# Performance work log

Hardware: AMD Instinct MI355X
Metric: run time of the kernel (lower is better)

## Reference

```python
import jax, jax.numpy as jnp
import numpy as np

N_NODES = 100000
N_EDGES = 800000
N_GRAPHS = 16
NFEAT = 128
NHID = 128
NCLASS = 2


def setup_inputs() -> dict:
    key = jax.random.key(0)
    k1, k2, k3, k4, k5, k6, k7 = jax.random.split(key, 7)
    x = jax.random.normal(k1, (N_NODES, NFEAT), dtype=jnp.float32)
    edge_index = jax.random.randint(k2, (2, N_EDGES), 0, N_NODES, dtype=jnp.int64)
    batch = jnp.sort(jax.random.randint(k3, (N_NODES,), 0, N_GRAPHS, dtype=jnp.int64))
    # GCNConv params (glorot-ish scale)
    W1 = jax.random.normal(k4, (NFEAT, NHID), dtype=jnp.float32) / np.sqrt(NFEAT)
    b1 = jnp.zeros((NHID,), dtype=jnp.float32)
    W2 = jax.random.normal(k5, (NHID, NCLASS), dtype=jnp.float32) / np.sqrt(NHID)
    b2 = jnp.zeros((NCLASS,), dtype=jnp.float32)
    return {"x": x, "edge_index": edge_index, "batch": batch,
            "W1": W1, "b1": b1, "W2": W2, "b2": b2}


def _prep_edges(edge_index, n):
    """Add self-loops and compute symmetric GCN normalization."""
    loop = jnp.arange(n, dtype=edge_index.dtype)
    row = jnp.concatenate([edge_index[0], loop])  # source
    col = jnp.concatenate([edge_index[1], loop])  # target
    deg = jax.ops.segment_sum(jnp.ones_like(col, dtype=jnp.float32), col, num_segments=n)
    dinv = jnp.where(deg > 0, jax.lax.rsqrt(deg), 0.0)
    norm = dinv[row] * dinv[col]  # [E+N]
    return row, col, norm


def _gcn_conv(x, row, col, norm, W, b):
    h = x @ W                                  # [N, out]
    msg = h[row] * norm[:, None]               # gather + scale, [E+N, out]
    out = jax.ops.segment_sum(msg, col, num_segments=x.shape[0])  # scatter-add
    return out + b


def reference(x, edge_index, batch, W1, b1, W2, b2):
    n = x.shape[0]
    row, col, norm = _prep_edges(edge_index, n)
    h = jax.nn.relu(_gcn_conv(x, row, col, norm, W1, b1))
    # dropout is identity at inference
    h = _gcn_conv(h, row, col, norm, W2, b2)
    # global_mean_pool over graph ids
    sums = jax.ops.segment_sum(h, batch, num_segments=N_GRAPHS)          # [G, nclass]
    cnts = jax.ops.segment_sum(jnp.ones((n,), h.dtype), batch, num_segments=N_GRAPHS)
    pooled = sums / jnp.maximum(cnts, 1.0)[:, None]
    return jax.nn.log_softmax(pooled, axis=1)
```

## Files before the change

kernel.cpp:

```cpp
#include <hip/hip_runtime.h>
#include <hip/hip_bf16.h>

#define N_NODES 100000
#define N_EDGES 800000
#define N_GRAPHS 16
#define NFEAT 128
#define NHID 128
#define NCLASS 2

#define GEMM_BLOCKS 512
#define N_CHUNKS (N_NODES / 16)

#define FILL_BINS 8
#define FILL_SLICES 128
#define FILL_BIN_W (N_NODES / FILL_BINS)
#define FILL_SLICE_E (N_EDGES / FILL_SLICES)

#define SLOT_CAP 64
#define ZROW N_NODES

#define P2E_BLOCKS 1024
#define P2E_TPB 256

typedef unsigned int uint32;
typedef __attribute__((ext_vector_type(8))) short short8;
typedef __attribute__((ext_vector_type(4))) float f32x4;
typedef __attribute__((ext_vector_type(2))) float f32x2;

__device__ __forceinline__ unsigned short f2bf(float f) {
  __hip_bfloat16 h = __float2bfloat16(f);
  unsigned short r;
  __builtin_memcpy(&r, &h, 2);
  return r;
}

__global__ __launch_bounds__(256) void k_fill(const int* __restrict__ ei,
                                              int* __restrict__ deg,
                                              int* __restrict__ slots,
                                              unsigned char* __restrict__ xw8) {
  if (blockIdx.x == 0 && threadIdx.x < 32)
    ((uint32*)(xw8 + (size_t)ZROW * 128))[threadIdx.x] = 0u;
  int bin = blockIdx.x & (FILL_BINS - 1);
  int slice = blockIdx.x >> 3;
  int lo = bin * FILL_BIN_W;
  int hi = lo + FILL_BIN_W;
  int e0 = slice * FILL_SLICE_E;
  int e1 = e0 + FILL_SLICE_E;
  for (int e = e0 + threadIdx.x; e < e1; e += 256) {
    int c = ei[N_EDGES + e];
    if (c >= lo && c < hi) {
      int r = ei[e];
      int p = atomicAdd(&deg[c], 1);
      if (p < SLOT_CAP) slots[(size_t)c * SLOT_CAP + p] = r;
    }
  }
}

__global__ __launch_bounds__(256, 2) void k_gemm_mfma(const float* __restrict__ x,
                                                      const float* __restrict__ W1,
                                                      const int* __restrict__ deg,
                                                      unsigned char* __restrict__ xw8) {
  __shared__ __align__(16) unsigned short Wt[128 * 136];
  int t = threadIdx.x;
  for (int i = t; i < 4096; i += 256) {
    float4 w4 = ((const float4*)W1)[i];
    int k = i >> 5;
    int n0 = (i & 31) * 4;
    Wt[(n0 + 0) * 136 + k] = f2bf(w4.x);
    Wt[(n0 + 1) * 136 + k] = f2bf(w4.y);
    Wt[(n0 + 2) * 136 + k] = f2bf(w4.z);
    Wt[(n0 + 3) * 136 + k] = f2bf(w4.w);
  }
  __syncthreads();

  int lane = t & 63;
  int c = lane & 15;
  int quad = lane >> 4;
  short8 b[4][8];
#pragma unroll
  for (int kt = 0; kt < 4; ++kt)
#pragma unroll
    for (int nt = 0; nt < 8; ++nt)
      b[kt][nt] = *(const short8*)&Wt[(nt * 16 + c) * 136 + kt * 32 + quad * 8];

  int wave = blockIdx.x * 4 + (t >> 6);
  for (int chunk = wave; chunk < N_CHUNKS; chunk += GEMM_BLOCKS * 4) {
    const float* xr = x + (size_t)(chunk * 16 + c) * 128 + quad * 8;
    short8 a[4];
#pragma unroll
    for (int kt = 0; kt < 4; ++kt) {
      float4 f0 = *(const float4*)(xr + kt * 32);
      float4 f1 = *(const float4*)(xr + kt * 32 + 4);
      short8 v;
      v[0] = (short)f2bf(f0.x); v[1] = (short)f2bf(f0.y);
      v[2] = (short)f2bf(f0.z); v[3] = (short)f2bf(f0.w);
      v[4] = (short)f2bf(f1.x); v[5] = (short)f2bf(f1.y);
      v[6] = (short)f2bf(f1.z); v[7] = (short)f2bf(f1.w);
      a[kt] = v;
    }
    f32x4 acc[8];
#pragma unroll
    for (int nt = 0; nt < 8; ++nt) acc[nt] = (f32x4)(0.f);
#pragma unroll
    for (int kt = 0; kt < 4; ++kt)
#pragma unroll
      for (int nt = 0; nt < 8; ++nt)
        acc[nt] = __builtin_amdgcn_mfma_f32_16x16x32_bf16(a[kt], b[kt][nt], acc[nt], 0, 0, 0);

    int rbase = chunk * 16 + quad * 4;
#pragma unroll
    for (int r = 0; r < 4; ++r) {
      float d = rsqrtf((float)deg[rbase + r] + 1.0f);
      int w0 = __builtin_amdgcn_cvt_pk_fp8_f32(acc[0][r] * d, acc[1][r] * d, 0, false);
      w0 = __builtin_amdgcn_cvt_pk_fp8_f32(acc[2][r] * d, acc[3][r] * d, w0, true);
      int w1 = __builtin_amdgcn_cvt_pk_fp8_f32(acc[4][r] * d, acc[5][r] * d, 0, false);
      w1 = __builtin_amdgcn_cvt_pk_fp8_f32(acc[6][r] * d, acc[7][r] * d, w1, true);
      uint2 st;
      st.x = (uint32)w0;
      st.y = (uint32)w1;
      *(uint2*)&xw8[(size_t)(rbase + r) * 128 + c * 8] = st;
    }
  }
}

__global__ __launch_bounds__(256) void k_conv1(const unsigned char* __restrict__ xw8,
                                               const int* __restrict__ slots,
                                               const int* __restrict__ deg,
                                               const float* __restrict__ b1,
                                               const float* __restrict__ W2,
                                               float2* __restrict__ h2) {
  int t = threadIdx.x;
  int lane = t & 63;
  int j = lane & 15;
  int gbase = lane & 48;
  int node = blockIdx.x * 16 + (t >> 4);

  size_t st = (size_t)node * SLOT_CAP;
  int cnt = min(deg[node], SLOT_CAP);

  int rj = (j == 0) ? node : ((j <= cnt) ? slots[st + j - 1] : ZROW);

  f32x2 acc2[4];
#pragma unroll
  for (int k = 0; k < 4; ++k) acc2[k] = (f32x2)(0.f);

  const uint2* rowp = (const uint2*)xw8;

#pragma unroll
  for (int i = 0; i < 16; ++i) {
    int r = __shfl(rj, gbase + i, 64);
    uint2 u = rowp[(size_t)r * 16 + j];
    acc2[0] += __builtin_amdgcn_cvt_pk_f32_fp8(u.x, false);
    acc2[1] += __builtin_amdgcn_cvt_pk_f32_fp8(u.x, true);
    acc2[2] += __builtin_amdgcn_cvt_pk_f32_fp8(u.y, false);
    acc2[3] += __builtin_amdgcn_cvt_pk_f32_fp8(u.y, true);
  }

  for (int s = 16; s <= cnt; s += 16) {
    int idx = s + j;
    int rj2 = (idx <= cnt) ? slots[st + idx - 1] : ZROW;
#pragma unroll
    for (int i = 0; i < 16; ++i) {
      int r = __shfl(rj2, gbase + i, 64);
      uint2 u = rowp[(size_t)r * 16 + j];
      acc2[0] += __builtin_amdgcn_cvt_pk_f32_fp8(u.x, false);
      acc2[1] += __builtin_amdgcn_cvt_pk_f32_fp8(u.x, true);
      acc2[2] += __builtin_amdgcn_cvt_pk_f32_fp8(u.y, false);
      acc2[3] += __builtin_amdgcn_cvt_pk_f32_fp8(u.y, true);
    }
  }

  float dc = rsqrtf((float)cnt + 1.0f);
  float q0 = 0.f, q1 = 0.f;
  const float2* W2v = (const float2*)W2;
#pragma unroll
  for (int k = 0; k < 8; ++k) {
    float a = acc2[k >> 1][k & 1];
    float ok = fmaxf(a * dc + b1[k * 16 + j], 0.f) * dc;
    float2 wv = W2v[k * 16 + j];
    q0 += ok * wv.x;
    q1 += ok * wv.y;
  }
#pragma unroll
  for (int m = 1; m < 16; m <<= 1) {
    q0 += __shfl_xor(q0, m, 64);
    q1 += __shfl_xor(q1, m, 64);
  }
  if (j == 0) h2[node] = make_float2(q0, q1);
}

__global__ __launch_bounds__(P2E_TPB) void k_pool_edges(const float2* __restrict__ h2,
                                                        const int* __restrict__ ei,
                                                        const int* __restrict__ batch,
                                                        const int* __restrict__ deg,
                                                        float* __restrict__ partials) {
  __shared__ float sacc[N_GRAPHS * 2];
  int t = threadIdx.x;
  if (t < N_GRAPHS * 2) sacc[t] = 0.f;
  __syncthreads();
  int tid = blockIdx.x * P2E_TPB + t;
  int stride = P2E_BLOCKS * P2E_TPB;
  for (int e = tid; e < N_EDGES; e += stride) {
    int r = ei[e];
    int c = ei[N_EDGES + e];
    float2 v = h2[r];
    float dc = rsqrtf((float)deg[c] + 1.0f);
    int g = batch[c];
    atomicAdd(&sacc[g * 2 + 0], v.x * dc);
    atomicAdd(&sacc[g * 2 + 1], v.y * dc);
  }
  for (int n = tid; n < N_NODES; n += stride) {
    float2 v = h2[n];
    float dn = rsqrtf((float)deg[n] + 1.0f);
    int g = batch[n];
    atomicAdd(&sacc[g * 2 + 0], v.x * dn);
    atomicAdd(&sacc[g * 2 + 1], v.y * dn);
  }
  __syncthreads();
  if (t < N_GRAPHS * 2)
    partials[(size_t)blockIdx.x * (N_GRAPHS * 2) + t] = sacc[t];
}

__global__ __launch_bounds__(256) void k_tail(const float* __restrict__ partials,
                                              const int* __restrict__ batch,
                                              const float* __restrict__ b2,
                                              float* __restrict__ out) {
  __shared__ float red[8];
  __shared__ int cntsh;
  int g = blockIdx.x;
  int t = threadIdx.x;
  if (t == 0) {
    int lo = 0, hi = N_NODES;
    while (lo < hi) { int m = (lo + hi) >> 1; if (batch[m] < g) lo = m + 1; else hi = m; }
    int b0 = lo;
    lo = 0; hi = N_NODES;
    while (lo < hi) { int m = (lo + hi) >> 1; if (batch[m] < g + 1) lo = m + 1; else hi = m; }
    cntsh = lo - b0;
  }
  float s0 = 0.f, s1 = 0.f;
  for (int b = t; b < P2E_BLOCKS; b += 256) {
    s0 += partials[(size_t)b * (N_GRAPHS * 2) + g * 2 + 0];
    s1 += partials[(size_t)b * (N_GRAPHS * 2) + g * 2 + 1];
  }
#pragma unroll
  for (int m = 1; m < 64; m <<= 1) {
    s0 += __shfl_xor(s0, m, 64);
    s1 += __shfl_xor(s1, m, 64);
  }
  int wv = t >> 6, ln = t & 63;
  if (ln == 0) { red[wv * 2] = s0; red[wv * 2 + 1] = s1; }
  __syncthreads();
  if (t == 0) {
    float p0 = red[0] + red[2] + red[4] + red[6];
    float p1 = red[1] + red[3] + red[5] + red[7];
    float cnt = fmaxf((float)cntsh, 1.0f);
    p0 = p0 / cnt + b2[0];
    p1 = p1 / cnt + b2[1];
    float m = fmaxf(p0, p1);
    float lse = m + logf(expf(p0 - m) + expf(p1 - m));
    out[g * 2 + 0] = p0 - lse;
    out[g * 2 + 1] = p1 - lse;
  }
}

static inline size_t align256(size_t x) { return (x + 255) & ~(size_t)255; }

extern "C" void kernel_launch(void* const* d_in, const int* in_sizes, int n_in,
                              void* d_out, int out_size, void* d_ws, size_t ws_size,
                              hipStream_t stream) {
  (void)in_sizes; (void)n_in; (void)out_size; (void)ws_size;
  const float* x  = (const float*)d_in[0];
  const int*   ei = (const int*)d_in[1];
  const int*   batch = (const int*)d_in[2];
  const float* W1 = (const float*)d_in[3];
  const float* b1 = (const float*)d_in[4];
  const float* W2 = (const float*)d_in[5];
  const float* b2 = (const float*)d_in[6];
  float* out = (float*)d_out;

  char* w = (char*)d_ws;
  size_t off = 0;
  unsigned char* xw8 = (unsigned char*)(w + off); off = align256(off + (size_t)(N_NODES + 1) * NHID);
  int* slots = (int*)(w + off);          off = align256(off + (size_t)N_NODES * SLOT_CAP * 4);
  float2* h2 = (float2*)(w + off);       off = align256(off + (size_t)N_NODES * sizeof(float2));
  float* partials = (float*)(w + off);   off = align256(off + (size_t)P2E_BLOCKS * N_GRAPHS * 2 * 4);
  int* deg = (int*)(w + off);            off = align256(off + (size_t)N_NODES * 4);

  hipMemsetAsync(deg, 0, (size_t)N_NODES * 4, stream);
  k_fill<<<FILL_BINS * FILL_SLICES, 256, 0, stream>>>(ei, deg, slots, xw8);
  k_gemm_mfma<<<GEMM_BLOCKS, 256, 0, stream>>>(x, W1, deg, xw8);
  k_conv1<<<N_NODES / 16, 256, 0, stream>>>(xw8, slots, deg, b1, W2, h2);
  k_pool_edges<<<P2E_BLOCKS, P2E_TPB, 0, stream>>>(h2, ei, batch, deg, partials);
  k_tail<<<N_GRAPHS, 256, 0, stream>>>(partials, batch, b2, out);
}
```

Before: 192.7 us.

## Fuse edge fill and feature GEMM into one concurrent kernel, move source normalization to gather

Merges the edge-bucketing fill kernel and the MFMA GEMM into a single launch where one third of the blocks run the GEMM and two thirds run the fill. Because the GEMM no longer needs final degrees, the source-side rsqrt(deg) scaling moves from the GEMM store into the conv1 gather, where each neighbour's degree is loaded and its factor shuffled. This removes a kernel boundary and lets the compute-bound GEMM overlap the atomic-bound fill. The cost is an extra degree load and a multiply per neighbour in conv1, plus fp8 quantization now applied before scaling, which can change precision slightly.

```diff
diff --git a/kernel.cpp b/kernel.cpp
--- a/kernel.cpp
+++ b/kernel.cpp
@@ -8,13 +8,15 @@
 #define NHID 128
 #define NCLASS 2
 
-#define GEMM_BLOCKS 512
 #define N_CHUNKS (N_NODES / 16)
 
 #define FILL_BINS 8
 #define FILL_SLICES 128
 #define FILL_BIN_W (N_NODES / FILL_BINS)
 #define FILL_SLICE_E (N_EDGES / FILL_SLICES)
+
+#define FUSE_BLOCKS 1536
+#define GEMM_VBLOCKS 512
 
 #define SLOT_CAP 64
 #define ZROW N_NODES
@@ -34,34 +36,39 @@
   return r;
 }
 
-__global__ __launch_bounds__(256) void k_fill(const int* __restrict__ ei,
-                                              int* __restrict__ deg,
-                                              int* __restrict__ slots,
-                                              unsigned char* __restrict__ xw8) {
-  if (blockIdx.x == 0 && threadIdx.x < 32)
-    ((uint32*)(xw8 + (size_t)ZROW * 128))[threadIdx.x] = 0u;
-  int bin = blockIdx.x & (FILL_BINS - 1);
-  int slice = blockIdx.x >> 3;
-  int lo = bin * FILL_BIN_W;
-  int hi = lo + FILL_BIN_W;
-  int e0 = slice * FILL_SLICE_E;
-  int e1 = e0 + FILL_SLICE_E;
-  for (int e = e0 + threadIdx.x; e < e1; e += 256) {
-    int c = ei[N_EDGES + e];
-    if (c >= lo && c < hi) {
-      int r = ei[e];
-      int p = atomicAdd(&deg[c], 1);
-      if (p < SLOT_CAP) slots[(size_t)c * SLOT_CAP + p] = r;
-    }
-  }
-}
-
-__global__ __launch_bounds__(256, 2) void k_gemm_mfma(const float* __restrict__ x,
+__global__ __launch_bounds__(256, 2) void k_fill_gemm(const int* __restrict__ ei,
+                                                      int* __restrict__ deg,
+                                                      int* __restrict__ slots,
+                                                      const float* __restrict__ x,
                                                       const float* __restrict__ W1,
-                                                      const int* __restrict__ deg,
                                                       unsigned char* __restrict__ xw8) {
   __shared__ __align__(16) unsigned short Wt[128 * 136];
+  int bid = blockIdx.x;
+  int role = bid % 3;
   int t = threadIdx.x;
+
+  if (role < 2) {
+    int fid = (bid / 3) * 2 + role;
+    if (fid == 0 && t < 32)
+      ((uint32*)(xw8 + (size_t)ZROW * 128))[t] = 0u;
+    int bin = fid & (FILL_BINS - 1);
+    int slice = fid >> 3;
+    int lo = bin * FILL_BIN_W;
+    int hi = lo + FILL_BIN_W;
+    int e0 = slice * FILL_SLICE_E;
+    int e1 = e0 + FILL_SLICE_E;
+    for (int e = e0 + t; e < e1; e += 256) {
+      int c = ei[N_EDGES + e];
+      if (c >= lo && c < hi) {
+        int r = ei[e];
+        int p = atomicAdd(&deg[c], 1);
+        if (p < SLOT_CAP) slots[(size_t)c * SLOT_CAP + p] = r;
+      }
+    }
+    return;
+  }
+
+  int gid = bid / 3;
   for (int i = t; i < 4096; i += 256) {
     float4 w4 = ((const float4*)W1)[i];
     int k = i >> 5;
@@ -83,8 +90,8 @@
     for (int nt = 0; nt < 8; ++nt)
       b[kt][nt] = *(const short8*)&Wt[(nt * 16 + c) * 136 + kt * 32 + quad * 8];
 
-  int wave = blockIdx.x * 4 + (t >> 6);
-  for (int chunk = wave; chunk < N_CHUNKS; chunk += GEMM_BLOCKS * 4) {
+  int wave = gid * 4 + (t >> 6);
+  for (int chunk = wave; chunk < N_CHUNKS; chunk += GEMM_VBLOCKS * 4) {
     const float* xr = x + (size_t)(chunk * 16 + c) * 128 + quad * 8;
     short8 a[4];
 #pragma unroll
@@ -110,11 +117,10 @@
     int rbase = chunk * 16 + quad * 4;
 #pragma unroll
     for (int r = 0; r < 4; ++r) {
-      float d = rsqrtf((float)deg[rbase + r] + 1.0f);
-      int w0 = __builtin_amdgcn_cvt_pk_fp8_f32(acc[0][r] * d, acc[1][r] * d, 0, false);
-      w0 = __builtin_amdgcn_cvt_pk_fp8_f32(acc[2][r] * d, acc[3][r] * d, w0, true);
-      int w1 = __builtin_amdgcn_cvt_pk_fp8_f32(acc[4][r] * d, acc[5][r] * d, 0, false);
-      w1 = __builtin_amdgcn_cvt_pk_fp8_f32(acc[6][r] * d, acc[7][r] * d, w1, true);
+      int w0 = __builtin_amdgcn_cvt_pk_fp8_f32(acc[0][r], acc[1][r], 0, false);
+      w0 = __builtin_amdgcn_cvt_pk_fp8_f32(acc[2][r], acc[3][r], w0, true);
+      int w1 = __builtin_amdgcn_cvt_pk_fp8_f32(acc[4][r], acc[5][r], 0, false);
+      w1 = __builtin_amdgcn_cvt_pk_fp8_f32(acc[6][r], acc[7][r], w1, true);
       uint2 st;
       st.x = (uint32)w0;
       st.y = (uint32)w1;
@@ -136,9 +142,12 @@
   int node = blockIdx.x * 16 + (t >> 4);
 
   size_t st = (size_t)node * SLOT_CAP;
-  int cnt = min(deg[node], SLOT_CAP);
+  int dn = deg[node];
+  int cnt = min(dn, SLOT_CAP);
 
   int rj = (j == 0) ? node : ((j <= cnt) ? slots[st + j - 1] : ZROW);
+  float dj = 0.0f;
+  if (j <= cnt) dj = rsqrtf((float)((j == 0) ? dn : deg[rj]) + 1.0f);
 
   f32x2 acc2[4];
 #pragma unroll
@@ -149,28 +158,34 @@
 #pragma unroll
   for (int i = 0; i < 16; ++i) {
     int r = __shfl(rj, gbase + i, 64);
+    float d = __shfl(dj, gbase + i, 64);
     uint2 u = rowp[(size_t)r * 16 + j];
-    acc2[0] += __builtin_amdgcn_cvt_pk_f32_fp8(u.x, false);
-    acc2[1] += __builtin_amdgcn_cvt_pk_f32_fp8(u.x, true);
-    acc2[2] += __builtin_amdgcn_cvt_pk_f32_fp8(u.y, false);
-    acc2[3] += __builtin_amdgcn_cvt_pk_f32_fp8(u.y, true);
+    f32x2 dd = {d, d};
+    acc2[0] += __builtin_amdgcn_cvt_pk_f32_fp8(u.x, false) * dd;
+    acc2[1] += __builtin_amdgcn_cvt_pk_f32_fp8(u.x, true) * dd;
+    acc2[2] += __builtin_amdgcn_cvt_pk_f32_fp8(u.y, false) * dd;
+    acc2[3] += __builtin_amdgcn_cvt_pk_f32_fp8(u.y, true) * dd;
   }
 
   for (int s = 16; s <= cnt; s += 16) {
     int idx = s + j;
     int rj2 = (idx <= cnt) ? slots[st + idx - 1] : ZROW;
+    float dj2 = 0.0f;
+    if (idx <= cnt) dj2 = rsqrtf((float)deg[rj2] + 1.0f);
 #pragma unroll
     for (int i = 0; i < 16; ++i) {
       int r = __shfl(rj2, gbase + i, 64);
+      float d = __shfl(dj2, gbase + i, 64);
       uint2 u = rowp[(size_t)r * 16 + j];
-      acc2[0] += __builtin_amdgcn_cvt_pk_f32_fp8(u.x, false);
-      acc2[1] += __builtin_amdgcn_cvt_pk_f32_fp8(u.x, true);
-      acc2[2] += __builtin_amdgcn_cvt_pk_f32_fp8(u.y, false);
-      acc2[3] += __builtin_amdgcn_cvt_pk_f32_fp8(u.y, true);
+      f32x2 dd = {d, d};
+      acc2[0] += __builtin_amdgcn_cvt_pk_f32_fp8(u.x, false) * dd;
+      acc2[1] += __builtin_amdgcn_cvt_pk_f32_fp8(u.x, true) * dd;
+      acc2[2] += __builtin_amdgcn_cvt_pk_f32_fp8(u.y, false) * dd;
+      acc2[3] += __builtin_amdgcn_cvt_pk_f32_fp8(u.y, true) * dd;
     }
   }
 
-  float dc = rsqrtf((float)cnt + 1.0f);
+  float dc = rsqrtf((float)dn + 1.0f);
   float q0 = 0.f, q1 = 0.f;
   const float2* W2v = (const float2*)W2;
 #pragma unroll
@@ -287,8 +302,7 @@
   int* deg = (int*)(w + off);            off = align256(off + (size_t)N_NODES * 4);
 
   hipMemsetAsync(deg, 0, (size_t)N_NODES * 4, stream);
-  k_fill<<<FILL_BINS * FILL_SLICES, 256, 0, stream>>>(ei, deg, slots, xw8);
-  k_gemm_mfma<<<GEMM_BLOCKS, 256, 0, stream>>>(x, W1, deg, xw8);
+  k_fill_gemm<<<FUSE_BLOCKS, 256, 0, stream>>>(ei, deg, slots, x, W1, xw8);
   k_conv1<<<N_NODES / 16, 256, 0, stream>>>(xw8, slots, deg, b1, W2, h2);
   k_pool_edges<<<P2E_BLOCKS, P2E_TPB, 0, stream>>>(h2, ei, batch, deg, partials);
   k_tail<<<N_GRAPHS, 256, 0, stream>>>(partials, batch, b2, out);
```

Result: slower. 216.0 us (+12.1%).
